# Kernel tuning notes

Hardware: AMD Instinct MI355X
Metric: run time of the kernel (lower is better)

The kernel has to match this reference:

```python
import jax, jax.numpy as jnp
import numpy as np

B, T, D, O = 4, 1024, 256, 256


def setup_inputs() -> dict:
    key = jax.random.key(0)
    kx, kw = jax.random.split(key)
    x = jax.random.normal(kx, (B, T, D), dtype=jnp.float32)
    # he_normal init: stddev = sqrt(2 / fan_in), stacked per-position kernels [T, D, O]
    W = jax.random.normal(kw, (T, D, O), dtype=jnp.float32) * np.sqrt(2.0 / D).astype(np.float32)
    return {"x": x, "W": W}


def reference(x, W):
    # Original loop: out[:, i, :] = mean_{t<=i} (x[:, t, :] @ W[i])
    # = (cumulative mean of x along T) @ per-position kernel W[i].
    t = x.shape[1]
    counts = jnp.arange(1, t + 1, dtype=x.dtype)[:, None]  # (T,1)
    cm = jnp.cumsum(x, axis=1) / counts                    # (B,T,D) cumulative mean
    return jnp.einsum('btd,tdo->bto', cm, W)               # (B,T,O)
```

## Files before the change

### kernel.cpp

```cpp
#include <hip/hip_runtime.h>

#define B_ 4
#define T_ 1024
#define D_ 256
#define O_ 256
#define NC 32
#define CL 32

typedef float v4f __attribute__((ext_vector_type(4)));

__global__ __launch_bounds__(256) void chunk_sums(const float* __restrict__ x,
                                                  float* __restrict__ S) {
    const int d  = threadIdx.x;
    const int bc = blockIdx.x;
    const int b  = bc / NC;
    const int c  = bc % NC;
    const float* xp = x + ((size_t)b * T_ + (size_t)c * CL) * D_ + d;
    float s = 0.f;
#pragma unroll
    for (int i = 0; i < CL; ++i) s += xp[(size_t)i * D_];
    S[((size_t)b * NC + c) * D_ + d] = s;
}

__global__ __launch_bounds__(256) void cumsum_mean(const float* __restrict__ x,
                                                   const float* __restrict__ S,
                                                   float* __restrict__ cm) {
    const int d  = threadIdx.x;
    const int bc = blockIdx.x;
    const int b  = bc / NC;
    const int c  = bc % NC;
    float off = 0.f;
#pragma unroll
    for (int cc = 0; cc < NC; ++cc) {
        const float v = S[((size_t)b * NC + cc) * D_ + d];
        off += (cc < c) ? v : 0.f;
    }
    const float* xp = x  + ((size_t)b * T_ + (size_t)c * CL) * D_ + d;
    float*       cp = cm + ((size_t)b * T_ + (size_t)c * CL) * D_ + d;
    float run = off;
#pragma unroll 4
    for (int i = 0; i < CL; ++i) {
        run += xp[(size_t)i * D_];
        const int t = c * CL + i;
        cp[(size_t)i * D_] = run / (float)(t + 1);
    }
}

__global__ __launch_bounds__(256) void gemm_t(const float* __restrict__ cm,
                                              const float* __restrict__ W,
                                              float* __restrict__ out) {
    const int t   = blockIdx.x;
    const int tid = threadIdx.x;
    const int dq  = tid >> 6;
    const int oq  = tid & 63;

    __shared__ float cml[D_][4];
    __shared__ v4f   part[4][4][64];

#pragma unroll
    for (int b = 0; b < 4; ++b)
        cml[tid][b] = cm[((size_t)b * T_ + t) * D_ + tid];
    __syncthreads();

    const v4f* Wp = (const v4f*)(W + ((size_t)t * D_ + (size_t)dq * 64) * O_) + oq;

    v4f a0 = (v4f)(0.f), a1 = (v4f)(0.f), a2 = (v4f)(0.f), a3 = (v4f)(0.f);

    v4f w[16];
#pragma unroll
    for (int j = 0; j < 8; ++j)
        w[j] = __builtin_nontemporal_load(Wp + (size_t)j * (O_ / 4));

#pragma unroll 1
    for (int dd = 0; dd < 64; dd += 16) {
#pragma unroll
        for (int j = 0; j < 8; ++j)
            w[8 + j] = __builtin_nontemporal_load(Wp + (size_t)(dd + 8 + j) * (O_ / 4));
#pragma unroll
        for (int j = 0; j < 8; ++j) {
            const v4f c4 = *(const v4f*)cml[dq * 64 + dd + j];
            a0 += c4.x * w[j]; a1 += c4.y * w[j]; a2 += c4.z * w[j]; a3 += c4.w * w[j];
        }
        if (dd + 16 < 64) {
#pragma unroll
            for (int j = 0; j < 8; ++j)
                w[j] = __builtin_nontemporal_load(Wp + (size_t)(dd + 16 + j) * (O_ / 4));
        }
#pragma unroll
        for (int j = 0; j < 8; ++j) {
            const v4f c4 = *(const v4f*)cml[dq * 64 + dd + 8 + j];
            a0 += c4.x * w[8 + j]; a1 += c4.y * w[8 + j];
            a2 += c4.z * w[8 + j]; a3 += c4.w * w[8 + j];
        }
    }

    part[dq][0][oq] = a0;
    part[dq][1][oq] = a1;
    part[dq][2][oq] = a2;
    part[dq][3][oq] = a3;
    __syncthreads();

    if (dq == 0) {
#pragma unroll
        for (int b = 0; b < 4; ++b) {
            v4f r = part[0][b][oq] + part[1][b][oq] + part[2][b][oq] + part[3][b][oq];
            __builtin_nontemporal_store(
                r, (v4f*)&out[((size_t)b * T_ + t) * O_ + (size_t)oq * 4]);
        }
    }
}

extern "C" void kernel_launch(void* const* d_in, const int* in_sizes, int n_in,
                              void* d_out, int out_size, void* d_ws, size_t ws_size,
                              hipStream_t stream) {
    const float* x = (const float*)d_in[0];
    const float* W = (const float*)d_in[1];
    float* out = (float*)d_out;

    float* cm = (float*)d_ws;
    float* S  = (float*)d_ws + (size_t)B_ * T_ * D_;

    chunk_sums <<<B_ * NC, 256, 0, stream>>>(x, S);
    cumsum_mean<<<B_ * NC, 256, 0, stream>>>(x, S, cm);
    gemm_t     <<<T_,      256, 0, stream>>>(cm, W, out);
}
```

Measured before the change: 344.9 us.

## Stream W tiles into LDS via async global_load_lds with double buffering

Rewrites the per-position GEMM so W rows are copied directly from global memory into a double-buffered LDS tile with global_load_lds. Each wave now handles one batch row across all D and reads W from shared memory, which removes the cross-wave partial-sum reduction. The intent is to overlap W streaming with compute and cut register pressure. It adds per-tile barriers and relies on hand-written vmcnt waits, and the cumulative-mean values are read from global memory per row instead of from a shared-memory copy.

```diff
diff --git a/kernel.cpp b/kernel.cpp
--- a/kernel.cpp
+++ b/kernel.cpp
@@ -6,6 +6,9 @@
 #define O_ 256
 #define NC 32
 #define CL 32
+
+#define TROWS 16
+#define NTILE (D_ / TROWS)
 
 typedef float v4f __attribute__((ext_vector_type(4)));
 
@@ -49,65 +52,54 @@
 __global__ __launch_bounds__(256) void gemm_t(const float* __restrict__ cm,
                                               const float* __restrict__ W,
                                               float* __restrict__ out) {
-    const int t   = blockIdx.x;
-    const int tid = threadIdx.x;
-    const int dq  = tid >> 6;
-    const int oq  = tid & 63;
+    const int t    = blockIdx.x;
+    const int tid  = threadIdx.x;
+    const int wv   = __builtin_amdgcn_readfirstlane(tid >> 6);
+    const int lane = tid & 63;
 
-    __shared__ float cml[D_][4];
-    __shared__ v4f   part[4][4][64];
+    __shared__ float tile[2][TROWS][O_];
 
+    const float* Wt  = W  + (size_t)t * D_ * O_;
+    const float* cmt = cm + ((size_t)wv * T_ + t) * D_;
+
+    auto stage = [&](int k) {
 #pragma unroll
-    for (int b = 0; b < 4; ++b)
-        cml[tid][b] = cm[((size_t)b * T_ + t) * D_ + tid];
-    __syncthreads();
+        for (int j = 0; j < 4; ++j) {
+            const float* g = Wt + ((size_t)k * TROWS + wv * 4 + j) * O_ + lane * 4;
+            float*       l = &tile[k & 1][wv * 4 + j][0];
+            __builtin_amdgcn_global_load_lds(
+                (const __attribute__((address_space(1))) unsigned int*)g,
+                (__attribute__((address_space(3))) unsigned int*)l,
+                16, 0, 0);
+        }
+    };
 
-    const v4f* Wp = (const v4f*)(W + ((size_t)t * D_ + (size_t)dq * 64) * O_) + oq;
+    v4f acc = (v4f)(0.f);
 
-    v4f a0 = (v4f)(0.f), a1 = (v4f)(0.f), a2 = (v4f)(0.f), a3 = (v4f)(0.f);
+    stage(0);
+#pragma unroll 1
+    for (int k = 0; k < NTILE; ++k) {
+        if (k + 1 < NTILE) {
+            stage(k + 1);
+            asm volatile("s_waitcnt vmcnt(4)" ::: "memory");
+        } else {
+            asm volatile("s_waitcnt vmcnt(0)" ::: "memory");
+        }
+        __builtin_amdgcn_sched_barrier(0);
+        __builtin_amdgcn_s_barrier();
+        __builtin_amdgcn_sched_barrier(0);
 
-    v4f w[16];
+        const float* cs = cmt + k * TROWS;
 #pragma unroll
-    for (int j = 0; j < 8; ++j)
-        w[j] = __builtin_nontemporal_load(Wp + (size_t)j * (O_ / 4));
-
-#pragma unroll 1
-    for (int dd = 0; dd < 64; dd += 16) {
-#pragma unroll
-        for (int j = 0; j < 8; ++j)
-            w[8 + j] = __builtin_nontemporal_load(Wp + (size_t)(dd + 8 + j) * (O_ / 4));
-#pragma unroll
-        for (int j = 0; j < 8; ++j) {
-            const v4f c4 = *(const v4f*)cml[dq * 64 + dd + j];
-            a0 += c4.x * w[j]; a1 += c4.y * w[j]; a2 += c4.z * w[j]; a3 += c4.w * w[j];
+        for (int r = 0; r < TROWS; ++r) {
+            const v4f w4 = *(const v4f*)&tile[k & 1][r][lane * 4];
+            acc += cs[r] * w4;
         }
-        if (dd + 16 < 64) {
-#pragma unroll
-            for (int j = 0; j < 8; ++j)
-                w[j] = __builtin_nontemporal_load(Wp + (size_t)(dd + 16 + j) * (O_ / 4));
-        }
-#pragma unroll
-        for (int j = 0; j < 8; ++j) {
-            const v4f c4 = *(const v4f*)cml[dq * 64 + dd + 8 + j];
-            a0 += c4.x * w[8 + j]; a1 += c4.y * w[8 + j];
-            a2 += c4.z * w[8 + j]; a3 += c4.w * w[8 + j];
-        }
+        __builtin_amdgcn_s_barrier();
     }
 
-    part[dq][0][oq] = a0;
-    part[dq][1][oq] = a1;
-    part[dq][2][oq] = a2;
-    part[dq][3][oq] = a3;
-    __syncthreads();
-
-    if (dq == 0) {
-#pragma unroll
-        for (int b = 0; b < 4; ++b) {
-            v4f r = part[0][b][oq] + part[1][b][oq] + part[2][b][oq] + part[3][b][oq];
-            __builtin_nontemporal_store(
-                r, (v4f*)&out[((size_t)b * T_ + t) * O_ + (size_t)oq * 4]);
-        }
-    }
+    __builtin_nontemporal_store(
+        acc, (v4f*)&out[((size_t)wv * T_ + t) * O_ + (size_t)lane * 4]);
 }
 
 extern "C" void kernel_launch(void* const* d_in, const int* in_sizes, int n_in,
```

New measurement: 369.8 us. +7.2%, slower.
